# Optimization experiments

Hardware: AMD Instinct MI355X
Metric: run time of the kernel (lower is better)

The kernel has to match this reference:

```python
import jax, jax.numpy as jnp
import numpy as np

FT = 0.2  # clip floor (init arg ft)

def _norm_mat(m):
    # matrix / (count of nonzeros along last dim + 1e-30)
    deg = jnp.sum(m != 0, axis=-1, keepdims=True).astype(m.dtype)
    return m / (deg + 1e-30)

def _l2n(x):
    return x / (jnp.linalg.norm(x, axis=-1, keepdims=True) + 1e-30)

def setup_inputs():
    B, L, D, H, O = 2, 2048, 64, 64, 128
    N = 2 * L
    ks = jax.random.split(jax.random.key(0), 30)
    u = lambda i, s: jax.random.uniform(ks[i], s, jnp.float32)
    g = lambda i, s: jax.random.normal(ks[i], s, jnp.float32) * 0.05
    inp = {}
    inp['word_outputs_0'] = g(0, (B, L, D))
    inp['word_outputs_1'] = g(1, (B, L, D))
    inp['node_hidden'] = g(2, (B, D))
    inp['op_embedding'] = g(3, (B, O, D))
    inp['word_exist_sequence'] = (u(4, (B, N)) < 0.8).astype(jnp.float32)
    inp['word_exist_matrix'] = (u(5, (B, N, N)) < 0.8).astype(jnp.float32)
    inp['word_operator'] = (u(6, (B, N, O)) < 0.02).astype(jnp.float32)
    inp['word_word'] = (u(7, (B, N, N)) < 0.01).astype(jnp.float32)
    inp['depend_0'] = (u(8, (B, L, L)) < 0.05).astype(jnp.float32)
    inp['depend_1'] = (u(9, (B, L, L)) < 0.05).astype(jnp.float32)
    inp['goal_word'] = u(10, (B, N))
    names = [('Wg', (D, H)), ('bg', (H,)), ('Wwk', (D, H)), ('bwk', (H,)),
             ('Wws', (D, H)), ('bws', (H,)), ('Wo', (D, D)), ('bo', (D,)),
             ('Wupd', (3 * H, D)), ('bupd', (D,)), ('Wf', (3 * H + D, D)), ('bf', (D,)),
             ('Wf2', (2 * D, D)), ('bf2', (D,)), ('Wout', (D, D)), ('bout', (D,))]
    for i, (nm, s) in enumerate(names):
        inp[nm] = g(11 + i, s)
    return inp

def _forward(w0, w1, nh, opE, wes, wem, wop, ww, d0, d1, gw,
             Wg, bg, Wwk, bwk, Wws, bws, Wo, bo, Wupd, bupd, Wf, bf, Wf2, bf2, Wout, bout):
    all_w = jnp.concatenate([w0, w1], axis=1)                      # [B,N,D]
    goal_trans = (nh @ Wg + bg)[:, None, :]                        # [B,1,H] (broadcast = expand)
    word_g = _l2n(goal_trans * gw[..., None])                      # [B,N,H]
    word_w_k = _l2n(jnp.matmul(_norm_mat(ww * wem), all_w @ Wwk + bwk))
    ws0 = jnp.matmul(_norm_mat(d0), w0 @ Wws + bws)
    ws1 = jnp.matmul(_norm_mat(d1), w1 @ Wws + bws)
    word_w_s = _l2n(jnp.concatenate([ws0, ws1], axis=1))           # [B,N,H]
    neigh = jnp.concatenate([word_g, word_w_k, word_w_s], axis=-1)  # [B,N,3H]
    forget = jax.nn.sigmoid(jnp.concatenate([all_w, word_g, word_w_k, word_w_s], axis=-1) @ Wf + bf)
    word_updated = jnp.maximum(forget, FT) * all_w + (1.0 - forget) * jax.nn.relu(neigh @ Wupd + bupd)
    adj_op = _norm_mat(jnp.swapaxes(wes[..., None] * wop, 1, 2))   # [B,O,N]
    word_op = jnp.matmul(adj_op, word_updated @ Wo + bo)           # [B,O,D]
    forget2 = jax.nn.sigmoid(jnp.concatenate([opE, word_op], axis=-1) @ Wf2 + bf2)
    op_out = jnp.maximum(forget2, FT) * opE + (1.0 - forget2) * jax.nn.relu(word_op @ Wout + bout)
    # original returns (split(word_updated), op_embedding); concat along node axis here
    return jnp.concatenate([word_updated, op_out], axis=1)         # [B,N+O,D]

def reference(word_outputs_0, word_outputs_1, node_hidden, op_embedding,
              word_exist_sequence, word_exist_matrix, word_operator, word_word,
              depend_0, depend_1, goal_word,
              Wg, bg, Wwk, bwk, Wws, bws, Wo, bo, Wupd, bupd, Wf, bf, Wf2, bf2, Wout, bout):
    return _forward(word_outputs_0, word_outputs_1, node_hidden, op_embedding,
                    word_exist_sequence, word_exist_matrix, word_operator, word_word,
                    depend_0, depend_1, goal_word,
                    Wg, bg, Wwk, bwk, Wws, bws, Wo, bo, Wupd, bupd, Wf, bf, Wf2, bf2, Wout, bout)
```

## Files before the change

### kernel.cpp

```cpp
#include <hip/hip_runtime.h>
#include <cstdint>

typedef unsigned short u16;
typedef unsigned long long u64;

__device__ __forceinline__ u16 f2b(float f){
  union { float f; uint32_t i; } v; v.f = f;
  uint32_t r = v.i + 0x7FFFu + ((v.i >> 16) & 1u);
  return (u16)(r >> 16);
}
__device__ __forceinline__ float b2f(u16 u){
  union { uint32_t i; float f; } v; v.i = ((uint32_t)u) << 16; return v.f;
}
__device__ __forceinline__ float sigmoidf(float x){ return 1.0f / (1.0f + __expf(-x)); }

__global__ __launch_bounds__(256) void k_bits(
    const float* __restrict__ ww, const float* __restrict__ wem,
    const float* __restrict__ d0, const float* __restrict__ d1,
    const float* __restrict__ wes, const float* __restrict__ wop,
    const float* __restrict__ w0, const float* __restrict__ w1,
    const float* __restrict__ nh, const float* __restrict__ Wg, const float* __restrict__ bg,
    const float* __restrict__ Wf, const float* __restrict__ Wupd, const float* __restrict__ Wo,
    u16* __restrict__ psumB, int* __restrict__ pcntB,
    u16* __restrict__ psumD, int* __restrict__ pcntD,
    u64* __restrict__ bitOp, float* __restrict__ ghat,
    uint32_t* __restrict__ pkWf, uint32_t* __restrict__ pkWu, uint32_t* __restrict__ pkWo){
  __shared__ int q[4][288];
  int tid = threadIdx.x, wave = tid >> 6, lane = tid & 63;
  int bid = blockIdx.x;
  if (bid >= 2048){
    if (bid >= 2304){
      int aux = bid - 2304;
      if (aux == 16){
        if (tid < 128){
          int b = tid >> 6, h = tid & 63;
          float g = bg[h];
          for (int d = 0; d < 64; ++d) g += nh[b*64 + d] * Wg[d*64 + h];
          float ss = g * g;
          #pragma unroll
          for (int o = 32; o > 0; o >>= 1) ss += __shfl_xor(ss, o, 64);
          ghat[b*64 + h] = g / (sqrtf(ss) + 1e-30f);
        }
        return;
      }
      for (int k = tid; k < 1024; k += 256){
        int i = aux*1024 + k;
        const float* src; uint32_t* dst; int li;
        if (i < 8192){ src = Wf; dst = pkWf; li = i; }
        else if (i < 14336){ src = Wupd; dst = pkWu; li = i - 8192; }
        else { src = Wo; dst = pkWo; li = i - 14336; }
        int k2 = li >> 6, ln = li & 63;
        dst[li] = (uint32_t)f2b(src[(2*k2)*64 + ln]) | ((uint32_t)f2b(src[(2*k2+1)*64 + ln]) << 16);
      }
      return;
    }
    int w = (bid - 2048)*4 + wave;
    int ng0 = w * 8;
    #pragma unroll
    for (int i = 0; i < 8; ++i){
      int n = ng0 + i;
      float vx = wop[(size_t)n*128 + lane];
      float vy = wop[(size_t)n*128 + 64 + lane];
      float e  = wes[n];
      u64 m0 = __ballot((e != 0.f) && (vx != 0.f));
      u64 m1 = __ballot((e != 0.f) && (vy != 0.f));
      if (lane == 0) bitOp[(size_t)n*2]     = m0;
      if (lane == 1) bitOp[(size_t)n*2 + 1] = m1;
    }
    return;
  }
  int wid = __builtin_amdgcn_readfirstlane(bid*4 + wave);
  float4 a0, a1, a2, a3, b0v, b1v, b2v, b3v;
#define ISSUE_MASKS(tt) { \
  int t_ = (tt); \
  if (t_ < 32768){ \
    int row_ = t_ >> 2, ch_ = t_ & 3; \
    const float4* ra_ = (const float4*)(ww  + (size_t)row_*4096 + ch_*1024) + lane; \
    const float4* rb_ = (const float4*)(wem + (size_t)row_*4096 + ch_*1024) + lane; \
    a0 = ra_[0]; a1 = ra_[64]; a2 = ra_[128]; a3 = ra_[192]; \
    b0v = rb_[0]; b1v = rb_[64]; b2v = rb_[128]; b3v = rb_[192]; \
  } else { \
    int idx_ = t_ - 32768, rowp_ = idx_ >> 1, ch_ = idx_ & 1; \
    const float* A_; \
    if (rowp_ < 4096) A_ = d0 + (size_t)rowp_*2048 + ch_*1024; \
    else { int rr_ = rowp_ - 4096; A_ = d1 + (size_t)rr_*2048 + ch_*1024; } \
    const float4* ra_ = (const float4*)A_ + lane; \
    a0 = ra_[0]; a1 = ra_[64]; a2 = ra_[128]; a3 = ra_[192]; \
  } }
  ISSUE_MASKS(wid)
  #pragma unroll 1
  for (int it = 0; it < 6; ++it){
    int t = wid + it*8192;
    bool big = (t < 32768);
    const float *sA, *sB;
    int jbase, thresh;
    u16* ps; int* pc;
    if (big){
      int row = t >> 2, chunk = t & 3;
      int b = row >> 12;
      sA = w0 + (size_t)b*131072;
      sB = w1 + (size_t)b*131072 - 131072;
      jbase = chunk*1024; thresh = 2048;
      ps = psumB + (size_t)t*64; pc = pcntB + t;
    } else {
      int idx = t - 32768, rowp = idx >> 1, chunk = idx & 1;
      if (rowp < 4096){ int b = rowp >> 11; sA = w0 + (size_t)b*131072; }
      else { int rr = rowp - 4096, b = rr >> 11; sA = w1 + (size_t)b*131072; }
      sB = sA;
      jbase = chunk*1024; thresh = 4096;
      ps = psumD + (size_t)idx*64; pc = pcntD + idx;
    }
    u64 myw = 0;
#define B4(i, va, vb) { \
  u64 m0 = __ballot((va.x != 0.f) && (!big || (vb.x != 0.f))); \
  u64 m1 = __ballot((va.y != 0.f) && (!big || (vb.y != 0.f))); \
  u64 m2 = __ballot((va.z != 0.f) && (!big || (vb.z != 0.f))); \
  u64 m3 = __ballot((va.w != 0.f) && (!big || (vb.w != 0.f))); \
  if (lane == (i)*4 + 0) myw = m0; \
  if (lane == (i)*4 + 1) myw = m1; \
  if (lane == (i)*4 + 2) myw = m2; \
  if (lane == (i)*4 + 3) myw = m3; }
    B4(0, a0, b0v) B4(1, a1, b1v) B4(2, a2, b2v) B4(3, a3, b3v)
#undef B4
    int c = __popcll(myw);
    int pre = c;
    #pragma unroll
    for (int off = 1; off < 64; off <<= 1){
      int tt = __shfl_up(pre, off, 64);
      if (lane >= off) pre += tt;
    }
    int total = __shfl(pre, 63, 64);
    int base = pre - c;
    int colhi = (lane >> 2) * 256 + (lane & 3);
    u64 m = myw;
    while (m){
      int p = __builtin_ctzll(m); m &= m - 1;
      q[wave][base++] = colhi + p*4;
    }
    int totP = (total + 15) & ~15;
    if (lane < totP - total) q[wave][total + lane] = 0;
    if (it < 5) ISSUE_MASKS(t + 8192)
    float acc = 0.f;
    int nb = totP >> 4;
    float g0[16], g1[16];
#define GISS(arr, bi) { int bse = (bi) << 4; \
  _Pragma("unroll") for (int k2 = 0; k2 < 16; ++k2){ \
    int j = __builtin_amdgcn_readfirstlane(jbase + q[wave][bse + k2]); \
    const float* pp = ((j < thresh) ? sA : sB) + (size_t)j*64; \
    arr[k2] = pp[lane]; } }
#define GACC(arr, bi) { int bse = (bi) << 4; \
  _Pragma("unroll") for (int k2 = 0; k2 < 16; ++k2) \
    acc += (bse + k2 < total) ? arr[k2] : 0.f; }
    if (nb > 0) GISS(g0, 0)
    for (int bi = 0; bi < nb; bi += 2){
      if (bi + 1 < nb) GISS(g1, bi + 1)
      GACC(g0, bi)
      if (bi + 1 < nb){
        if (bi + 2 < nb) GISS(g0, bi + 2)
        GACC(g1, bi + 1)
      }
    }
#undef GISS
#undef GACC
    ps[lane] = f2b(acc);
    if (lane == 0) pc[0] = total;
  }
#undef ISSUE_MASKS
}

__global__ __launch_bounds__(256, 2) void k_mid(
    const u16* __restrict__ psumB, const int* __restrict__ pcntB,
    const u16* __restrict__ psumD, const int* __restrict__ pcntD,
    const float* __restrict__ Wwk, const float* __restrict__ bwk,
    const float* __restrict__ Wws, const float* __restrict__ bws,
    const float* __restrict__ w0, const float* __restrict__ w1,
    const float* __restrict__ gw, const float* __restrict__ ghat,
    const uint32_t* __restrict__ pkWf, const uint32_t* __restrict__ pkWu,
    const uint32_t* __restrict__ pkWo,
    const float* __restrict__ bf, const float* __restrict__ bupd, const float* __restrict__ bo,
    float* __restrict__ out, float* __restrict__ WUo){
  __shared__ uint32_t ldsU[16384];
  __shared__ float xsh[4][256];
  int tid = threadIdx.x, lane = tid & 63, wave = tid >> 6;
  float* sWk = (float*)ldsU;
  float* sWs = (float*)ldsU + 4096;
  for (int i = tid; i < 1024; i += 256){
    ((float4*)sWk)[i] = ((const float4*)Wwk)[i];
    ((float4*)sWs)[i] = ((const float4*)Wws)[i];
  }
  __syncthreads();
  float bwkL = bwk[lane], bwsL = bws[lane];
  float wk[4], wsv[4], aw[4], wgv[4];
  #pragma unroll
  for (int t = 0; t < 4; ++t){
    int row = blockIdx.x*4 + wave + t*2048;
    int b = row >> 12, n = row & 4095;
    float S = b2f(psumB[((size_t)row*4 + 0)*64 + lane]) + b2f(psumB[((size_t)row*4 + 1)*64 + lane])
            + b2f(psumB[((size_t)row*4 + 2)*64 + lane]) + b2f(psumB[((size_t)row*4 + 3)*64 + lane]);
    int T = pcntB[row*4] + pcntB[row*4 + 1] + pcntB[row*4 + 2] + pcntB[row*4 + 3];
    float y = (float)T * bwkL;
    #pragma unroll 8
    for (int d = 0; d < 64; ++d) y += __shfl(S, d, 64) * sWk[d*64 + lane];
    float ss = y * y;
    #pragma unroll
    for (int o = 32; o > 0; o >>= 1) ss += __shfl_xor(ss, o, 64);
    wk[t] = y / (sqrtf(ss) + 1e-30f);
    int rp = (n < 2048) ? (b*2048 + n) : (4096 + b*2048 + (n - 2048));
    float S2 = b2f(psumD[((size_t)rp*2 + 0)*64 + lane]) + b2f(psumD[((size_t)rp*2 + 1)*64 + lane]);
    int T2 = pcntD[rp*2] + pcntD[rp*2 + 1];
    float y2 = (float)T2 * bwsL;
    #pragma unroll 8
    for (int d = 0; d < 64; ++d) y2 += __shfl(S2, d, 64) * sWs[d*64 + lane];
    float ss2 = y2 * y2;
    #pragma unroll
    for (int o = 32; o > 0; o >>= 1) ss2 += __shfl_xor(ss2, o, 64);
    wsv[t] = y2 / (sqrtf(ss2) + 1e-30f);
    aw[t] = (n < 2048) ? w0[((size_t)(b*2048 + n))*64 + lane]
                       : w1[((size_t)(b*2048 + n - 2048))*64 + lane];
    wgv[t] = (gw[b*4096 + n] != 0.f) ? ghat[b*64 + lane] : 0.f;
  }
  __syncthreads();
  uint32_t* pWf = ldsU;
  uint32_t* pWu = ldsU + 8192;
  uint32_t* pWo = ldsU + 14336;
  for (int i = tid; i < 2048; i += 256) ((uint4*)pWf)[i] = ((const uint4*)pkWf)[i];
  for (int i = tid; i < 1536; i += 256) ((uint4*)pWu)[i] = ((const uint4*)pkWu)[i];
  for (int i = tid; i < 512;  i += 256) ((uint4*)pWo)[i] = ((const uint4*)pkWo)[i];
  __syncthreads();
  float bff = bf[lane], bup = bupd[lane], boo = bo[lane];
  #pragma unroll
  for (int t = 0; t < 4; ++t){
    int row = blockIdx.x*4 + wave + t*2048;
    int b = row >> 12, n = row & 4095;
    xsh[wave][lane] = aw[t]; xsh[wave][64 + lane] = wgv[t];
    xsh[wave][128 + lane] = wk[t]; xsh[wave][192 + lane] = wsv[t];
    float f = bff, u = bup;
    #pragma unroll 8
    for (int k2 = 0; k2 < 32; ++k2){
      float2 xv = *(const float2*)&xsh[wave][2*k2];
      uint32_t wf = pWf[k2*64 + lane];
      f += xv.x * b2f((u16)wf) + xv.y * b2f((u16)(wf >> 16));
    }
    #pragma unroll 8
    for (int k2 = 32; k2 < 128; ++k2){
      float2 xv = *(const float2*)&xsh[wave][2*k2];
      uint32_t wf = pWf[k2*64 + lane];
      uint32_t wu = pWu[(k2 - 32)*64 + lane];
      f += xv.x * b2f((u16)wf) + xv.y * b2f((u16)(wf >> 16));
      u += xv.x * b2f((u16)wu) + xv.y * b2f((u16)(wu >> 16));
    }
    f = sigmoidf(f);
    u = fmaxf(u, 0.f);
    float wu = fmaxf(f, 0.2f) * aw[t] + (1.f - f) * u;
    out[((size_t)b*4224 + n)*64 + lane] = wu;
    float o = boo;
    #pragma unroll 8
    for (int k2 = 0; k2 < 32; ++k2){
      uint32_t wo2 = pWo[k2*64 + lane];
      o += __shfl(wu, 2*k2, 64) * b2f((u16)wo2) + __shfl(wu, 2*k2 + 1, 64) * b2f((u16)(wo2 >> 16));
    }
    WUo[(size_t)row*64 + lane] = o;
  }
}

__global__ __launch_bounds__(256) void k_opfin(
    const u64* __restrict__ bitOp, const float* __restrict__ WUo,
    const float* __restrict__ opE,
    const float* __restrict__ Wf2, const float* __restrict__ bf2,
    const float* __restrict__ Wout, const float* __restrict__ bout,
    float* __restrict__ out){
  __shared__ float sW2[8192];
  __shared__ float sWo[4096];
  __shared__ int q[4][96];
  __shared__ float sacc[4][64];
  __shared__ int scnt[4];
  __shared__ float xsh[128];
  int tid = threadIdx.x, lane = tid & 63, wave = tid >> 6;
  for (int i = tid; i < 2048; i += 256) ((float4*)sW2)[i] = ((const float4*)Wf2)[i];
  for (int i = tid; i < 1024; i += 256) ((float4*)sWo)[i] = ((const float4*)Wout)[i];
  int rowIdx = blockIdx.x;
  int b = rowIdx >> 7, o = rowIdx & 127;
  int wrd = o >> 6, bit = o & 63;
  const u64* bp = bitOp + (size_t)b*8192 + (size_t)wave*2048 + wrd;
  u64 lt = (1ULL << lane) - 1ULL;
  u64 vv[16];
  #pragma unroll
  for (int it = 0; it < 16; ++it) vv[it] = bp[(size_t)(it*64 + lane)*2];
  int cnt = 0;
  #pragma unroll
  for (int it = 0; it < 16; ++it){
    bool nz = (vv[it] >> bit) & 1ULL;
    u64 m = __ballot(nz);
    if (nz) q[wave][cnt + (int)__popcll(m & lt)] = wave*1024 + it*64 + lane;
    cnt += (int)__popcll(m);
  }
  const float* Xb = WUo + (size_t)b*4096*64 + lane;
  float acc = 0.f;
  int i = 0;
  for (; i + 8 <= cnt; i += 8){
    int4 c0 = *(const int4*)&q[wave][i];
    int4 c1 = *(const int4*)&q[wave][i + 4];
    float v0 = Xb[(size_t)c0.x*64], v1 = Xb[(size_t)c0.y*64];
    float v2 = Xb[(size_t)c0.z*64], v3 = Xb[(size_t)c0.w*64];
    float v4 = Xb[(size_t)c1.x*64], v5 = Xb[(size_t)c1.y*64];
    float v6 = Xb[(size_t)c1.z*64], v7 = Xb[(size_t)c1.w*64];
    acc += ((v0 + v1) + (v2 + v3)) + ((v4 + v5) + (v6 + v7));
  }
  for (; i < cnt; ++i) acc += Xb[(size_t)q[wave][i]*64];
  sacc[wave][lane] = acc;
  if (lane == 0) scnt[wave] = cnt;
  __syncthreads();
  if (wave == 0){
    float t = sacc[0][lane] + sacc[1][lane] + sacc[2][lane] + sacc[3][lane];
    float deg = (float)(scnt[0] + scnt[1] + scnt[2] + scnt[3]);
    float wo = t / (deg + 1e-30f);
    float e  = opE[(size_t)rowIdx*64 + lane];
    xsh[lane] = e; xsh[64 + lane] = wo;
    float f = bf2[lane], u = bout[lane];
    #pragma unroll 8
    for (int k = 0; k < 128; ++k) f += xsh[k] * sW2[k*64 + lane];
    #pragma unroll 8
    for (int d = 0; d < 64; ++d)  u += xsh[64 + d] * sWo[d*64 + lane];
    f = sigmoidf(f);
    u = fmaxf(u, 0.f);
    float res = fmaxf(f, 0.2f) * e + (1.f - f) * u;
    out[((size_t)b*4224 + 4096 + o)*64 + lane] = res;
  }
}

extern "C" void kernel_launch(void* const* d_in, const int* in_sizes, int n_in,
                              void* d_out, int out_size, void* d_ws, size_t ws_size,
                              hipStream_t stream){
  const float* w0   = (const float*)d_in[0];
  const float* w1   = (const float*)d_in[1];
  const float* nh   = (const float*)d_in[2];
  const float* opE  = (const float*)d_in[3];
  const float* wes  = (const float*)d_in[4];
  const float* wem  = (const float*)d_in[5];
  const float* wop  = (const float*)d_in[6];
  const float* ww   = (const float*)d_in[7];
  const float* d0   = (const float*)d_in[8];
  const float* d1   = (const float*)d_in[9];
  const float* gw   = (const float*)d_in[10];
  const float* Wg   = (const float*)d_in[11];
  const float* bg   = (const float*)d_in[12];
  const float* Wwk  = (const float*)d_in[13];
  const float* bwk  = (const float*)d_in[14];
  const float* Wws  = (const float*)d_in[15];
  const float* bws  = (const float*)d_in[16];
  const float* Wo   = (const float*)d_in[17];
  const float* bo   = (const float*)d_in[18];
  const float* Wupd = (const float*)d_in[19];
  const float* bupd = (const float*)d_in[20];
  const float* Wf   = (const float*)d_in[21];
  const float* bf   = (const float*)d_in[22];
  const float* Wf2  = (const float*)d_in[23];
  const float* bf2  = (const float*)d_in[24];
  const float* Wout = (const float*)d_in[25];
  const float* bout = (const float*)d_in[26];

  float* ws    = (float*)d_ws;
  float* ghat  = ws;
  uint32_t* pkWf = (uint32_t*)(ws + 128);
  uint32_t* pkWu = (uint32_t*)(ws + 8320);
  uint32_t* pkWo = (uint32_t*)(ws + 14464);
  u64*  bitOp  = (u64*)(ws + 16512);
  u16*  psumB  = (u16*)(ws + 49280);
  int*  pcntB  = (int*)(ws + 1097856);
  u16*  psumD  = (u16*)(ws + 1130624);
  int*  pcntD  = (int*)(ws + 1654912);
  float* WUo   = ws + 2195584;
  float* out   = (float*)d_out;

  k_bits<<<2321, 256, 0, stream>>>(ww, wem, d0, d1, wes, wop, w0, w1,
                                   nh, Wg, bg, Wf, Wupd, Wo,
                                   psumB, pcntB, psumD, pcntD,
                                   bitOp, ghat, pkWf, pkWu, pkWo);
  k_mid<<<512, 256, 0, stream>>>(psumB, pcntB, psumD, pcntD,
                                 Wwk, bwk, Wws, bws, w0, w1, gw, ghat,
                                 pkWf, pkWu, pkWo, bf, bupd, bo, out, WUo);
  k_opfin<<<256, 256, 0, stream>>>(bitOp, WUo, opE, Wf2, bf2, Wout, bout, out);
}
```

Baseline: 437.7 us.

## Pre-pack word features to bf16 and gather two rows per wave load

Adds a prep kernel that converts w0/w1 into a packed bf16 table indexed by the concatenated node id. The sparse gather in k_bits then reads 32-bit words holding two bf16 values. Each half-wave handles a different neighbour row, so one wave load covers two rows at half the bytes, and the halves are combined with a cross-lane shuffle. This targets gather bandwidth and issue count. The cost is an extra launch, an extra workspace buffer, and bf16 rounding of inputs before summation.

```diff
diff --git a/kernel.cpp b/kernel.cpp
--- a/kernel.cpp
+++ b/kernel.cpp
@@ -14,11 +14,38 @@
 }
 __device__ __forceinline__ float sigmoidf(float x){ return 1.0f / (1.0f + __expf(-x)); }
 
+__global__ __launch_bounds__(256) void k_prep(
+    const float* __restrict__ w0, const float* __restrict__ w1,
+    uint32_t* __restrict__ wpk){
+  int tid = threadIdx.x, blk = blockIdx.x;
+  int b = blk >> 6;
+  int j = (blk & 63) * 64 + (tid >> 2);
+  int part = tid & 3;
+  const float* src = (j < 2048) ? (w0 + ((size_t)(b*2048 + j))*64 + part*16)
+                                : (w1 + ((size_t)(b*2048 + j - 2048))*64 + part*16);
+  uint32_t* dst = wpk + ((size_t)b*4096 + j)*32 + part*8;
+  float4 v0 = ((const float4*)src)[0];
+  float4 v1 = ((const float4*)src)[1];
+  float4 v2 = ((const float4*)src)[2];
+  float4 v3 = ((const float4*)src)[3];
+  uint4 o0, o1;
+  o0.x = (uint32_t)f2b(v0.x) | ((uint32_t)f2b(v0.y) << 16);
+  o0.y = (uint32_t)f2b(v0.z) | ((uint32_t)f2b(v0.w) << 16);
+  o0.z = (uint32_t)f2b(v1.x) | ((uint32_t)f2b(v1.y) << 16);
+  o0.w = (uint32_t)f2b(v1.z) | ((uint32_t)f2b(v1.w) << 16);
+  o1.x = (uint32_t)f2b(v2.x) | ((uint32_t)f2b(v2.y) << 16);
+  o1.y = (uint32_t)f2b(v2.z) | ((uint32_t)f2b(v2.w) << 16);
+  o1.z = (uint32_t)f2b(v3.x) | ((uint32_t)f2b(v3.y) << 16);
+  o1.w = (uint32_t)f2b(v3.z) | ((uint32_t)f2b(v3.w) << 16);
+  ((uint4*)dst)[0] = o0;
+  ((uint4*)dst)[1] = o1;
+}
+
 __global__ __launch_bounds__(256) void k_bits(
     const float* __restrict__ ww, const float* __restrict__ wem,
     const float* __restrict__ d0, const float* __restrict__ d1,
     const float* __restrict__ wes, const float* __restrict__ wop,
-    const float* __restrict__ w0, const float* __restrict__ w1,
+    const uint32_t* __restrict__ wpk,
     const float* __restrict__ nh, const float* __restrict__ Wg, const float* __restrict__ bg,
     const float* __restrict__ Wf, const float* __restrict__ Wupd, const float* __restrict__ Wo,
     u16* __restrict__ psumB, int* __restrict__ pcntB,
@@ -69,7 +96,7 @@
     }
     return;
   }
-  int wid = __builtin_amdgcn_readfirstlane(bid*4 + wave);
+  int wid = bid*4 + wave;
   float4 a0, a1, a2, a3, b0v, b1v, b2v, b3v;
 #define ISSUE_MASKS(tt) { \
   int t_ = (tt); \
@@ -88,26 +115,24 @@
     a0 = ra_[0]; a1 = ra_[64]; a2 = ra_[128]; a3 = ra_[192]; \
   } }
   ISSUE_MASKS(wid)
+  int half = lane >> 5, dcol = lane & 31;
   #pragma unroll 1
   for (int it = 0; it < 6; ++it){
     int t = wid + it*8192;
     bool big = (t < 32768);
-    const float *sA, *sB;
-    int jbase, thresh;
+    const uint32_t* wub;
     u16* ps; int* pc;
     if (big){
       int row = t >> 2, chunk = t & 3;
       int b = row >> 12;
-      sA = w0 + (size_t)b*131072;
-      sB = w1 + (size_t)b*131072 - 131072;
-      jbase = chunk*1024; thresh = 2048;
+      wub = wpk + (size_t)b*131072 + (size_t)(chunk*1024)*32 + dcol;
       ps = psumB + (size_t)t*64; pc = pcntB + t;
     } else {
       int idx = t - 32768, rowp = idx >> 1, chunk = idx & 1;
-      if (rowp < 4096){ int b = rowp >> 11; sA = w0 + (size_t)b*131072; }
-      else { int rr = rowp - 4096, b = rr >> 11; sA = w1 + (size_t)b*131072; }
-      sB = sA;
-      jbase = chunk*1024; thresh = 4096;
+      int b, jadd = chunk*1024;
+      if (rowp < 4096){ b = rowp >> 11; }
+      else { int rr = rowp - 4096; b = rr >> 11; jadd += 2048; }
+      wub = wpk + (size_t)b*131072 + (size_t)jadd*32 + dcol;
       ps = psumD + (size_t)idx*64; pc = pcntD + idx;
     }
     u64 myw = 0;
@@ -137,20 +162,22 @@
       int p = __builtin_ctzll(m); m &= m - 1;
       q[wave][base++] = colhi + p*4;
     }
-    int totP = (total + 15) & ~15;
+    int totP = (total + 31) & ~31;
     if (lane < totP - total) q[wave][total + lane] = 0;
     if (it < 5) ISSUE_MASKS(t + 8192)
-    float acc = 0.f;
-    int nb = totP >> 4;
-    float g0[16], g1[16];
-#define GISS(arr, bi) { int bse = (bi) << 4; \
+    float accE = 0.f, accO = 0.f;
+    int nb = totP >> 5;
+    uint32_t g0[16], g1[16];
+#define GISS(arr, bi) { int bse = (bi) << 5; \
   _Pragma("unroll") for (int k2 = 0; k2 < 16; ++k2){ \
-    int j = __builtin_amdgcn_readfirstlane(jbase + q[wave][bse + k2]); \
-    const float* pp = ((j < thresh) ? sA : sB) + (size_t)j*64; \
-    arr[k2] = pp[lane]; } }
-#define GACC(arr, bi) { int bse = (bi) << 4; \
-  _Pragma("unroll") for (int k2 = 0; k2 < 16; ++k2) \
-    acc += (bse + k2 < total) ? arr[k2] : 0.f; }
+    int j = q[wave][bse + 2*k2 + half]; \
+    arr[k2] = wub[(size_t)j*32]; } }
+#define GACC(arr, bi) { int bse = (bi) << 5; \
+  _Pragma("unroll") for (int k2 = 0; k2 < 16; ++k2){ \
+    bool v = (bse + 2*k2 + half) < total; \
+    uint32_t wv = arr[k2]; \
+    accE += v ? b2f((u16)wv) : 0.f; \
+    accO += v ? b2f((u16)(wv >> 16)) : 0.f; } }
     if (nb > 0) GISS(g0, 0)
     for (int bi = 0; bi < nb; bi += 2){
       if (bi + 1 < nb) GISS(g1, bi + 1)
@@ -162,7 +189,10 @@
     }
 #undef GISS
 #undef GACC
-    ps[lane] = f2b(acc);
+    accE += __shfl_xor(accE, 32, 64);
+    accO += __shfl_xor(accO, 32, 64);
+    if (lane < 32)
+      ((uint32_t*)ps)[lane] = (uint32_t)f2b(accE) | ((uint32_t)f2b(accO) << 16);
     if (lane == 0) pc[0] = total;
   }
 #undef ISSUE_MASKS
@@ -370,9 +400,11 @@
   u16*  psumD  = (u16*)(ws + 1130624);
   int*  pcntD  = (int*)(ws + 1654912);
   float* WUo   = ws + 2195584;
+  uint32_t* wpk = (uint32_t*)(ws + 2719872);
   float* out   = (float*)d_out;
 
-  k_bits<<<2321, 256, 0, stream>>>(ww, wem, d0, d1, wes, wop, w0, w1,
+  k_prep<<<128, 256, 0, stream>>>(w0, w1, wpk);
+  k_bits<<<2321, 256, 0, stream>>>(ww, wem, d0, d1, wes, wop, wpk,
                                    nh, Wg, bg, Wf, Wupd, Wo,
                                    psumB, pcntB, psumD, pcntD,
                                    bitOp, ghat, pkWf, pkWu, pkWo);
```

Result: no change. 431.1 us (-1.5%).
